# Kernel optimization log

Hardware: AMD Instinct MI355X
Metric: run time of the kernel (lower is better)

## Reference

```python
import jax, jax.numpy as jnp
import numpy as np

IN_FEATURES = 4096
OUT_FEATURES = 4096
N_TOKENS = 1024

@jax.custom_vjp
def binarize(w):
    # UnipolarSte.forward: (w > 0).float()
    return (w > 0).astype(w.dtype)

def _bin_fwd(w):
    return binarize(w), None

def _bin_bwd(_, g):
    # UnipolarSte.backward: F.hardtanh(grad_output) == clip(g, -1, 1)
    return (jnp.clip(g, -1.0, 1.0),)

binarize.defvjp(_bin_fwd, _bin_bwd)

def setup_inputs() -> dict:
    key = jax.random.key(0)
    kx, kw = jax.random.split(key)
    x = jax.random.normal(kx, (N_TOKENS, IN_FEATURES), dtype=jnp.float32)
    weight = jax.random.normal(kw, (OUT_FEATURES, IN_FEATURES), dtype=jnp.float32)
    scaling_factor = jnp.ones((OUT_FEATURES,), dtype=jnp.float32)
    return {"x": x, "weight": weight, "scaling_factor": scaling_factor}

def reference(x, weight, scaling_factor):
    w_b = binarize(weight)                      # [out, in] in {0,1}
    out = jnp.einsum('ni,oi->no', x, w_b)       # F.linear(x, w_b)
    # s_eff = round(clamp(s,1)).detach() - s.detach() + s
    s_round = jax.lax.stop_gradient(jnp.round(jnp.clip(scaling_factor, 1.0, None)))
    s_eff = s_round - jax.lax.stop_gradient(scaling_factor) + scaling_factor
    return out * s_eff[None, :]
```

## Files before the change

### kernel.cpp

```cpp
#include <hip/hip_runtime.h>

#define M_TOK 1024
#define NOUT  4096
#define KIN   4096

typedef __attribute__((ext_vector_type(8))) short bf16x8_t;
typedef __attribute__((ext_vector_type(4))) float f32x4_t;


__device__ __forceinline__ unsigned pack_bf16(float a, float b) {
  unsigned ua = __float_as_uint(a);
  unsigned ub = __float_as_uint(b);
  ua = (ua + 0x7FFFu + ((ua >> 16) & 1u)) >> 16;
  ub = (ub + 0x7FFFu + ((ub >> 16) & 1u)) >> 16;
  return ua | (ub << 16);
}

__global__ __launch_bounds__(256) void prep_wx(const float* __restrict__ w,
                                               unsigned short* __restrict__ bfrag,
                                               const float4* __restrict__ x4,
                                               uint4* __restrict__ xfrag) {
  __shared__ unsigned long long lbits[16][17];
  const int tid  = threadIdx.x;
  const int lane = tid & 63;
  const int wave = tid >> 6;

  if (blockIdx.x < 1024) {
    const int n16 = blockIdx.x >> 2;
    const int kq  = blockIdx.x & 3;
#pragma unroll 1
    for (int rr = 0; rr < 16; ++rr) {
      const float* wr = w + (size_t)(n16 * 16 + rr) * KIN + kq * 1024 + wave * 256;
      unsigned long long mine = 0;
#pragma unroll
      for (int q = 0; q < 4; ++q) {
        float v = wr[q * 64 + lane];
        unsigned long long m = __ballot(v > 0.f);
        if (lane == q) mine = m;
      }
      if (lane < 4) lbits[rr][wave * 4 + lane] = mine;
    }
    __syncthreads();
#pragma unroll
    for (int it = 0; it < 4; ++it) {
      const int idx = it * 256 + tid;
      const int l = idx & 63, ktl = idx >> 6;
      const unsigned long long w64 = lbits[l & 15][ktl];
      const int quad = l >> 4;
      const unsigned b0 = (unsigned)(w64 >> (quad * 8)) & 0xFFu;
      const unsigned b1 = (unsigned)(w64 >> (quad * 8 + 32)) & 0xFFu;
      bfrag[((size_t)n16 * 64 + kq * 16 + ktl) * 64 + l] =
          (unsigned short)(b0 | (b1 << 8));
    }
  } else {
    const unsigned t = (blockIdx.x - 1024) * 256 + tid;
    const int l = t & 63;
    const unsigned f = t >> 6;
    const int m16 = f >> 7, k32 = f & 127;
    const int row = m16 * 16 + (l & 15);
    const int c4  = k32 * 8 + (l >> 4) * 2;
    const float4* p = x4 + (size_t)row * (KIN / 4) + c4;
    float4 a = p[0], b = p[1];
    uint4 o;
    o.x = pack_bf16(a.x, a.y);
    o.y = pack_bf16(a.z, a.w);
    o.z = pack_bf16(b.x, b.y);
    o.w = pack_bf16(b.z, b.w);
    xfrag[t] = o;
  }
}

__global__ __launch_bounds__(256, 2) void gemm_bin_kernel(
    const unsigned short* __restrict__ Xf,
    const unsigned short* __restrict__ Bf,
    const float* __restrict__ sf,
    float* __restrict__ C) {
  const int tid  = threadIdx.x;
  const int lane = tid & 63;
  const int wave = tid >> 6;
  const int quad = lane >> 4;
  const int l16  = lane & 15;
  const unsigned bid = blockIdx.x;
  const int xcd = bid & 7, idx = bid >> 3;
  const int m0 = (xcd * 2 + (idx >> 5)) * 64;
  const int n0 = (idx & 31) * 128;
  const int wn = wave * 32;
  const int m16b = m0 >> 4;
  const int n16b = (n0 + wn) >> 4;

  const uint4* Xf4 = (const uint4*)Xf;

  f32x4_t acc[4][2];
#pragma unroll
  for (int i = 0; i < 4; ++i)
#pragma unroll
    for (int j = 0; j < 2; ++j)
      acc[i][j] = (f32x4_t){0.f, 0.f, 0.f, 0.f};

  uint4 a[2][4][2];
  unsigned b[2][2];

  auto LOAD = [&](int u, int kt) {
#pragma unroll
    for (int i = 0; i < 4; ++i)
#pragma unroll
      for (int ks = 0; ks < 2; ++ks)
        a[u][i][ks] = Xf4[((size_t)(m16b + i) * 128 + kt * 2 + ks) * 64 + lane];
#pragma unroll
    for (int j = 0; j < 2; ++j)
      b[u][j] = (unsigned)Bf[((n16b + j) * 64 + kt) * 64 + lane];
  };

  auto COMP = [&](int u) {
#pragma unroll
    for (int j = 0; j < 2; ++j)
#pragma unroll
      for (int ks = 0; ks < 2; ++ks) {
        const unsigned br = b[u][j];
        union { unsigned u32[4]; bf16x8_t v; } ex;
#pragma unroll
        for (int p = 0; p < 4; ++p)
          ex.u32[p] = ((br << (14 - 8 * ks - 2 * p)) |
                       (br << (29 - 8 * ks - 2 * p))) & 0x40004000u;
#pragma unroll
        for (int i = 0; i < 4; ++i) {
          union { uint4 q; bf16x8_t v; } av;
          av.q = a[u][i][ks];
          acc[i][j] = __builtin_amdgcn_mfma_f32_16x16x32_bf16(av.v, ex.v, acc[i][j], 0, 0, 0);
        }
      }
  };

  LOAD(0, 0);
  for (int kt = 0; kt < 64; kt += 2) {
    LOAD(1, kt + 1);
    COMP(0);
    if (kt + 2 < 64) LOAD(0, kt + 2);
    COMP(1);
  }

#pragma unroll
  for (int j = 0; j < 2; ++j) {
    const int n = n0 + wn + j * 16 + l16;
    const float s = rintf(fmaxf(sf[n], 1.0f)) * 0.5f;
#pragma unroll
    for (int i = 0; i < 4; ++i) {
      const int mr = m0 + i * 16 + quad * 4;
#pragma unroll
      for (int r = 0; r < 4; ++r)
        C[(size_t)(mr + r) * NOUT + n] = acc[i][j][r] * s;
    }
  }
}

extern "C" void kernel_launch(void* const* d_in, const int* in_sizes, int n_in,
                              void* d_out, int out_size, void* d_ws, size_t ws_size,
                              hipStream_t stream) {
  const float* x  = (const float*)d_in[0];
  const float* w  = (const float*)d_in[1];
  const float* sf = (const float*)d_in[2];
  float* out = (float*)d_out;

  unsigned short* Bfrag = (unsigned short*)d_ws;
  unsigned short* Xfrag = (unsigned short*)((char*)d_ws + (4u << 20));

  prep_wx<<<3072, 256, 0, stream>>>(w, Bfrag, (const float4*)x, (uint4*)Xfrag);
  gemm_bin_kernel<<<512, 256, 0, stream>>>(Xfrag, Bfrag, sf, out);
}
```

Measured before the change: 149.7 us.

## Pack weight bits per-thread with float4 loads and emit exact 1.0 bf16

The weight binarization pass now has each thread read float4 vectors and build its 16-bit fragment directly, replacing the ballot plus shared-memory transpose. The bit layout changes to consecutive k per byte, so the GEMM's bf16 expansion is rewritten to produce 1.0 (0x3F80) through a multiply instead of 2.0, and the 0.5 epilogue scale is removed. This aims to cut prep-kernel cost from shuffles, LDS and the barrier, at the price of more blocks and strided per-thread loads, plus a multiply in the inner loop.

```diff
diff --git a/kernel.cpp b/kernel.cpp
--- a/kernel.cpp
+++ b/kernel.cpp
@@ -16,44 +16,31 @@
   return ua | (ub << 16);
 }
 
-__global__ __launch_bounds__(256) void prep_wx(const float* __restrict__ w,
+__device__ __forceinline__ unsigned bits8(float4 a, float4 b) {
+  return  (unsigned)(a.x > 0.f)        | ((unsigned)(a.y > 0.f) << 1) |
+         ((unsigned)(a.z > 0.f) << 2)  | ((unsigned)(a.w > 0.f) << 3) |
+         ((unsigned)(b.x > 0.f) << 4)  | ((unsigned)(b.y > 0.f) << 5) |
+         ((unsigned)(b.z > 0.f) << 6)  | ((unsigned)(b.w > 0.f) << 7);
+}
+
+__global__ __launch_bounds__(256) void prep_wx(const float4* __restrict__ w4,
                                                unsigned short* __restrict__ bfrag,
                                                const float4* __restrict__ x4,
                                                uint4* __restrict__ xfrag) {
-  __shared__ unsigned long long lbits[16][17];
-  const int tid  = threadIdx.x;
-  const int lane = tid & 63;
-  const int wave = tid >> 6;
-
-  if (blockIdx.x < 1024) {
-    const int n16 = blockIdx.x >> 2;
-    const int kq  = blockIdx.x & 3;
-#pragma unroll 1
-    for (int rr = 0; rr < 16; ++rr) {
-      const float* wr = w + (size_t)(n16 * 16 + rr) * KIN + kq * 1024 + wave * 256;
-      unsigned long long mine = 0;
-#pragma unroll
-      for (int q = 0; q < 4; ++q) {
-        float v = wr[q * 64 + lane];
-        unsigned long long m = __ballot(v > 0.f);
-        if (lane == q) mine = m;
-      }
-      if (lane < 4) lbits[rr][wave * 4 + lane] = mine;
-    }
-    __syncthreads();
-#pragma unroll
-    for (int it = 0; it < 4; ++it) {
-      const int idx = it * 256 + tid;
-      const int l = idx & 63, ktl = idx >> 6;
-      const unsigned long long w64 = lbits[l & 15][ktl];
-      const int quad = l >> 4;
-      const unsigned b0 = (unsigned)(w64 >> (quad * 8)) & 0xFFu;
-      const unsigned b1 = (unsigned)(w64 >> (quad * 8 + 32)) & 0xFFu;
-      bfrag[((size_t)n16 * 64 + kq * 16 + ktl) * 64 + l] =
-          (unsigned short)(b0 | (b1 << 8));
-    }
+  const unsigned bb = blockIdx.x;
+  if (bb < 4096) {
+    const unsigned t = bb * 256 + threadIdx.x;
+    const int l16 = t & 15, quad = (t >> 4) & 3;
+    const int kt = (t >> 6) & 63, n16 = t >> 12;
+    const int n = n16 * 16 + l16;
+    const float4* p = w4 + (size_t)n * (KIN / 4) + kt * 16 + quad * 2;
+    float4 f0 = p[0], f1 = p[1];
+    float4 f2 = p[8], f3 = p[9];
+    const unsigned b0 = bits8(f0, f1);
+    const unsigned b1 = bits8(f2, f3);
+    bfrag[t] = (unsigned short)(b0 | (b1 << 8));
   } else {
-    const unsigned t = (blockIdx.x - 1024) * 256 + tid;
+    const unsigned t = (bb - 4096) * 256 + threadIdx.x;
     const int l = t & 63;
     const unsigned f = t >> 6;
     const int m16 = f >> 7, k32 = f & 127;
@@ -116,12 +103,13 @@
     for (int j = 0; j < 2; ++j)
 #pragma unroll
       for (int ks = 0; ks < 2; ++ks) {
-        const unsigned br = b[u][j];
+        unsigned byte = (b[u][j] >> (ks * 8)) & 0xFFu;
         union { unsigned u32[4]; bf16x8_t v; } ex;
 #pragma unroll
-        for (int p = 0; p < 4; ++p)
-          ex.u32[p] = ((br << (14 - 8 * ks - 2 * p)) |
-                       (br << (29 - 8 * ks - 2 * p))) & 0x40004000u;
+        for (int p = 0; p < 4; ++p) {
+          unsigned tt = (byte >> (2 * p)) & 3u;
+          ex.u32[p] = ((tt | (tt << 15)) & 0x10001u) * 0x3F80u;
+        }
 #pragma unroll
         for (int i = 0; i < 4; ++i) {
           union { uint4 q; bf16x8_t v; } av;
@@ -142,7 +130,7 @@
 #pragma unroll
   for (int j = 0; j < 2; ++j) {
     const int n = n0 + wn + j * 16 + l16;
-    const float s = rintf(fmaxf(sf[n], 1.0f)) * 0.5f;
+    const float s = rintf(fmaxf(sf[n], 1.0f));
 #pragma unroll
     for (int i = 0; i < 4; ++i) {
       const int mr = m0 + i * 16 + quad * 4;
@@ -164,6 +152,7 @@
   unsigned short* Bfrag = (unsigned short*)d_ws;
   unsigned short* Xfrag = (unsigned short*)((char*)d_ws + (4u << 20));
 
-  prep_wx<<<3072, 256, 0, stream>>>(w, Bfrag, (const float4*)x, (uint4*)Xfrag);
+  prep_wx<<<6144, 256, 0, stream>>>((const float4*)w, Bfrag, (const float4*)x,
+                                    (uint4*)Xfrag);
   gemm_bin_kernel<<<512, 256, 0, stream>>>(Xfrag, Bfrag, sf, out);
 }
```

After: 145.4 us. 2.9% less time.
